# Kernel optimization log

Hardware: AMD Instinct MI355X
Metric: run time of the kernel (lower is better)

## Reference

```python
import jax, jax.numpy as jnp
import numpy as np

INPUT_SIZE = 256
N_DIM = 128
BATCH = 1024


def setup_inputs() -> dict:
    key = jax.random.key(0)
    ks = jax.random.split(key, 8)
    X = jax.random.normal(ks[0], (BATCH, INPUT_SIZE), dtype=jnp.float32)
    h = jax.random.normal(ks[1], (BATCH, INPUT_SIZE * N_DIM), dtype=jnp.float32)
    W_r = jax.random.normal(ks[2], (INPUT_SIZE, 1, N_DIM), dtype=jnp.float32)
    W_z = jax.random.normal(ks[3], (INPUT_SIZE, 1, N_DIM), dtype=jnp.float32)
    W_h = jax.random.normal(ks[4], (INPUT_SIZE, 1, N_DIM), dtype=jnp.float32)
    # orthogonal init for U (matches nn.init.orthogonal_ in spirit)
    def ortho(k):
        a = jax.random.normal(k, (INPUT_SIZE, N_DIM, N_DIM), dtype=jnp.float32)
        q, _ = jnp.linalg.qr(a)
        return q.astype(jnp.float32)
    U_r = ortho(ks[5])
    U_z = ortho(ks[6])
    U_h = ortho(ks[7])
    b_r = jnp.zeros((INPUT_SIZE, N_DIM), dtype=jnp.float32)
    b_z = jnp.zeros((INPUT_SIZE, N_DIM), dtype=jnp.float32)
    b_h = jnp.zeros((INPUT_SIZE, N_DIM), dtype=jnp.float32)
    return {"X": X, "h": h, "W_r": W_r, "W_z": W_z, "W_h": W_h,
            "U_r": U_r, "U_z": U_z, "U_h": U_h,
            "b_r": b_r, "b_z": b_z, "b_h": b_h}


def reference(X, h, W_r, W_z, W_h, U_r, U_z, U_h, b_r, b_z, b_h):
    B = X.shape[0]
    hg = h.reshape(B, INPUT_SIZE, N_DIM)  # [B, I, D]
    # X contribution: X[b,i] * W[i,0,k] -> [B, I, D]
    xW_r = X[:, :, None] * W_r[:, 0, :][None]
    xW_z = X[:, :, None] * W_z[:, 0, :][None]
    xW_h = X[:, :, None] * W_h[:, 0, :][None]
    # grouped GEMMs: [B,I,D] x [I,D,D] -> [B,I,D]
    r = jax.nn.sigmoid(xW_r + jnp.einsum('bij,ijk->bik', hg, U_r) + b_r)
    z = jax.nn.sigmoid(xW_z + jnp.einsum('bij,ijk->bik', hg, U_z) + b_z)
    h_tilde = jnp.tanh(xW_h + jnp.einsum('bij,ijk->bik', r * hg, U_h) + b_h)
    h_new = z * hg + (1.0 - z) * h_tilde
    return (h_new.reshape(B, INPUT_SIZE * N_DIM),
            h_tilde.reshape(B, INPUT_SIZE * N_DIM))
```

## Files before the change

### kernel.cpp

```cpp
#include <hip/hip_runtime.h>
#include <hip/hip_bf16.h>
#include <stdint.h>

#define I_SIZE 256
#define D_DIM 128
#define BATCH 1024

typedef __attribute__((ext_vector_type(8))) short short8;
typedef __attribute__((ext_vector_type(4))) short short4v;
typedef __attribute__((ext_vector_type(4))) float floatx4;

__device__ inline short f2bf(float f) {
    union { float f; uint32_t u; } v; v.f = f;
    uint32_t u = v.u;
    uint32_t r = (u + 0x7FFFu + ((u >> 16) & 1u)) >> 16;
    return (short)(r & 0xFFFFu);
}
__device__ inline float bf2f(short s) {
    union { uint32_t u; float f; } v; v.u = ((uint32_t)(uint16_t)s) << 16;
    return v.f;
}
__device__ inline uint32_t pkbf(float a, float b) {
    __hip_bfloat162 h = __float22bfloat162_rn(make_float2(a, b));
    union { __hip_bfloat162 h; uint32_t u; } v; v.h = h; return v.u;
}
__device__ inline float sigmoidf_fast(float x) { return 1.0f / (1.0f + __expf(-x)); }
__device__ inline float tanhf_fast(float x)    { return 2.0f / (1.0f + __expf(-2.0f * x)) - 1.0f; }

#define S_H 136

__global__ __launch_bounds__(1024, 4) void gru_fused(
    const float* __restrict__ X, const float* __restrict__ H,
    const float* __restrict__ Wr, const float* __restrict__ Wz, const float* __restrict__ Wh,
    const float* __restrict__ Ur, const float* __restrict__ Uz, const float* __restrict__ Uh,
    const float* __restrict__ br, const float* __restrict__ bz, const float* __restrict__ bh,
    float* __restrict__ out)
{
    __shared__ short Ut[3 * D_DIM * D_DIM];
    __shared__ short hgb[D_DIM * S_H];
    __shared__ float Wl[6][D_DIM];

    const int tid   = threadIdx.x;
    const int group = blockIdx.x;
    const int lane  = tid & 63;
    const int w     = tid >> 6;

    if (tid < D_DIM) {
        Wl[0][tid] = Wr[group * D_DIM + tid];
        Wl[1][tid] = Wz[group * D_DIM + tid];
        Wl[2][tid] = Wh[group * D_DIM + tid];
        Wl[3][tid] = br[group * D_DIM + tid];
        Wl[4][tid] = bz[group * D_DIM + tid];
        Wl[5][tid] = bh[group * D_DIM + tid];
    }

    {
        const int kc = tid & 127;
        const int jb = tid >> 7;
        #pragma unroll
        for (int g = 0; g < 3; ++g) {
            const float* Ug = ((g == 0) ? Ur : (g == 1) ? Uz : Uh)
                              + (size_t)group * (D_DIM * D_DIM);
            short* dst = &Ut[g * (D_DIM * D_DIM)];
            #pragma unroll
            for (int m = 0; m < 4; ++m) {
                const int j0 = m * 8 + jb;
                float a0 = Ug[(4 * j0 + 0) * D_DIM + kc];
                float a1 = Ug[(4 * j0 + 1) * D_DIM + kc];
                float a2 = Ug[(4 * j0 + 2) * D_DIM + kc];
                float a3 = Ug[(4 * j0 + 3) * D_DIM + kc];
                short4v s; s.x = f2bf(a0); s.y = f2bf(a1); s.z = f2bf(a2); s.w = f2bf(a3);
                const int p = (j0 >> 1) ^ (kc & 7);
                *(short4v*)&dst[kc * D_DIM + p * 8 + 4 * (j0 & 1)] = s;
            }
        }
    }

    const int am = lane & 15;
    const int aq = lane >> 4;
    const int rg = w >> 1;
    const int nh = w & 1;
    const int r0 = rg * 16;
    const size_t HOFF = (size_t)BATCH * I_SIZE * D_DIM;
    const int srow = tid >> 3;
    const int scol = (tid & 7) * 4;

    int pswz[4];
    #pragma unroll
    for (int kk = 0; kk < 4; ++kk) pswz[kk] = ((4 * kk + aq) ^ (am & 7)) * 8;

    const floatx4 zero = {0.f, 0.f, 0.f, 0.f};

    for (int pass = 0; pass < 8; ++pass) {
        const int R = pass * 128;

        #pragma unroll
        for (int it = 0; it < 4; ++it) {
            int col = scol + it * 32;
            float4 v = *(const float4*)(H + (size_t)(R + srow) * (I_SIZE * D_DIM)
                                        + group * D_DIM + col);
            uint2 uu; uu.x = pkbf(v.x, v.y); uu.y = pkbf(v.z, v.w);
            *(uint2*)&hgb[srow * S_H + col] = uu;
        }
        __syncthreads();

        short8 a[4];
        #pragma unroll
        for (int kk = 0; kk < 4; ++kk)
            a[kk] = *(const short8*)&hgb[(r0 + am) * S_H + kk * 32 + aq * 8];

        floatx4 accr[4], accz[4];
        #pragma unroll
        for (int t2 = 0; t2 < 4; ++t2) { accr[t2] = zero; accz[t2] = zero; }

        #pragma unroll
        for (int t2 = 0; t2 < 4; ++t2) {
            const int n = nh * 64 + t2 * 16 + am;
            const short* rowp = &Ut[n * D_DIM];
            #pragma unroll
            for (int kk = 0; kk < 4; ++kk)
                accr[t2] = __builtin_amdgcn_mfma_f32_16x16x32_bf16(
                    a[kk], *(const short8*)(rowp + pswz[kk]), accr[t2], 0, 0, 0);
            #pragma unroll
            for (int kk = 0; kk < 4; ++kk)
                accz[t2] = __builtin_amdgcn_mfma_f32_16x16x32_bf16(
                    a[kk], *(const short8*)(rowp + 16384 + pswz[kk]), accz[t2], 0, 0, 0);
        }

        float Xv[4];
        #pragma unroll
        for (int pp = 0; pp < 4; ++pp)
            Xv[pp] = X[(size_t)(R + r0 + aq * 4 + pp) * I_SIZE + group];

        float zr[4][4], hgc[4][4];
        #pragma unroll
        for (int t2 = 0; t2 < 4; ++t2) {
            const int c = nh * 64 + t2 * 16 + am;
            const float wr = Wl[0][c], wz = Wl[1][c], brv = Wl[3][c], bzv = Wl[4][c];
            #pragma unroll
            for (int pp = 0; pp < 4; ++pp) {
                const int rl = r0 + aq * 4 + pp;
                float hgv = bf2f(hgb[rl * S_H + c]);
                float rv = sigmoidf_fast(accr[t2][pp] + Xv[pp] * wr + brv);
                float zv = sigmoidf_fast(accz[t2][pp] + Xv[pp] * wz + bzv);
                zr[t2][pp]  = zv;
                hgc[t2][pp] = hgv;
                hgb[rl * S_H + c] = f2bf(rv * hgv);
            }
        }
        __syncthreads();

        short8 ap[4];
        #pragma unroll
        for (int kk = 0; kk < 4; ++kk)
            ap[kk] = *(const short8*)&hgb[(r0 + am) * S_H + kk * 32 + aq * 8];

        floatx4 acch[4];
        #pragma unroll
        for (int t2 = 0; t2 < 4; ++t2) acch[t2] = zero;
        #pragma unroll
        for (int t2 = 0; t2 < 4; ++t2) {
            const int n = nh * 64 + t2 * 16 + am;
            const short* rowp = &Ut[32768 + n * D_DIM];
            #pragma unroll
            for (int kk = 0; kk < 4; ++kk)
                acch[t2] = __builtin_amdgcn_mfma_f32_16x16x32_bf16(
                    ap[kk], *(const short8*)(rowp + pswz[kk]), acch[t2], 0, 0, 0);
        }

        #pragma unroll
        for (int t2 = 0; t2 < 4; ++t2) {
            const int c = nh * 64 + t2 * 16 + am;
            const float wh = Wl[2][c], bhv = Wl[5][c];
            #pragma unroll
            for (int pp = 0; pp < 4; ++pp) {
                const int rl = r0 + aq * 4 + pp;
                float ht = tanhf_fast(acch[t2][pp] + Xv[pp] * wh + bhv);
                float zv = zr[t2][pp];
                float hn = zv * hgc[t2][pp] + (1.0f - zv) * ht;
                size_t o = (size_t)(R + rl) * (I_SIZE * D_DIM) + group * D_DIM + c;
                out[o]        = hn;
                out[HOFF + o] = ht;
            }
        }
        __syncthreads();
    }
}

extern "C" void kernel_launch(void* const* d_in, const int* in_sizes, int n_in,
                              void* d_out, int out_size, void* d_ws, size_t ws_size,
                              hipStream_t stream) {
    const float* X  = (const float*)d_in[0];
    const float* H  = (const float*)d_in[1];
    const float* Wr = (const float*)d_in[2];
    const float* Wz = (const float*)d_in[3];
    const float* Wh = (const float*)d_in[4];
    const float* Ur = (const float*)d_in[5];
    const float* Uz = (const float*)d_in[6];
    const float* Uh = (const float*)d_in[7];
    const float* br = (const float*)d_in[8];
    const float* bz = (const float*)d_in[9];
    const float* bh = (const float*)d_in[10];

    (void)d_ws; (void)ws_size;

    gru_fused<<<dim3(I_SIZE), dim3(1024), 0, stream>>>(
        X, H, Wr, Wz, Wh, Ur, Uz, Uh, br, bz, bh, (float*)d_out);
}
```

Baseline: 462.2 us.

## Prefetch next H tile into registers and use LDS-only barriers

Loads the next pass's 128 rows of H into registers before the r/z MFMAs, so the global load latency overlaps with compute, and writes them to shared memory at the end of each pass. Caches the block's column of X in shared memory once instead of doing strided global loads every pass. Replaces __syncthreads with an inline-asm barrier that waits only on LDS counters, so outstanding global stores and prefetch loads do not stall the barrier. This raises register pressure through the held float4 prefetch, and the hand-written barrier depends on the compiler placing its vmcnt waits correctly.

```diff
diff --git a/kernel.cpp b/kernel.cpp
--- a/kernel.cpp
+++ b/kernel.cpp
@@ -26,6 +26,8 @@
 }
 __device__ inline float sigmoidf_fast(float x) { return 1.0f / (1.0f + __expf(-x)); }
 __device__ inline float tanhf_fast(float x)    { return 2.0f / (1.0f + __expf(-2.0f * x)) - 1.0f; }
+
+#define BAR_LGKM() asm volatile("s_waitcnt lgkmcnt(0)\n\ts_barrier" ::: "memory")
 
 #define S_H 136
 
@@ -39,6 +41,7 @@
     __shared__ short Ut[3 * D_DIM * D_DIM];
     __shared__ short hgb[D_DIM * S_H];
     __shared__ float Wl[6][D_DIM];
+    __shared__ float Xl[BATCH];
 
     const int tid   = threadIdx.x;
     const int group = blockIdx.x;
@@ -53,6 +56,7 @@
         Wl[4][tid] = bz[group * D_DIM + tid];
         Wl[5][tid] = bh[group * D_DIM + tid];
     }
+    Xl[tid] = X[(size_t)tid * I_SIZE + group];
 
     {
         const int kc = tid & 127;
@@ -76,14 +80,25 @@
         }
     }
 
+    const int srow = tid >> 3;
+    const int scol = (tid & 7) * 4;
+
+    #pragma unroll
+    for (int it = 0; it < 4; ++it) {
+        int col = scol + it * 32;
+        float4 v = *(const float4*)(H + (size_t)srow * (I_SIZE * D_DIM)
+                                    + group * D_DIM + col);
+        uint2 uu; uu.x = pkbf(v.x, v.y); uu.y = pkbf(v.z, v.w);
+        *(uint2*)&hgb[srow * S_H + col] = uu;
+    }
+    BAR_LGKM();
+
     const int am = lane & 15;
     const int aq = lane >> 4;
     const int rg = w >> 1;
     const int nh = w & 1;
     const int r0 = rg * 16;
     const size_t HOFF = (size_t)BATCH * I_SIZE * D_DIM;
-    const int srow = tid >> 3;
-    const int scol = (tid & 7) * 4;
 
     int pswz[4];
     #pragma unroll
@@ -94,20 +109,20 @@
     for (int pass = 0; pass < 8; ++pass) {
         const int R = pass * 128;
 
-        #pragma unroll
-        for (int it = 0; it < 4; ++it) {
-            int col = scol + it * 32;
-            float4 v = *(const float4*)(H + (size_t)(R + srow) * (I_SIZE * D_DIM)
-                                        + group * D_DIM + col);
-            uint2 uu; uu.x = pkbf(v.x, v.y); uu.y = pkbf(v.z, v.w);
-            *(uint2*)&hgb[srow * S_H + col] = uu;
-        }
-        __syncthreads();
-
         short8 a[4];
         #pragma unroll
         for (int kk = 0; kk < 4; ++kk)
             a[kk] = *(const short8*)&hgb[(r0 + am) * S_H + kk * 32 + aq * 8];
+
+        float4 pf[4];
+        if (pass < 7) {
+            #pragma unroll
+            for (int it = 0; it < 4; ++it) {
+                int col = scol + it * 32;
+                pf[it] = *(const float4*)(H + (size_t)(R + 128 + srow) * (I_SIZE * D_DIM)
+                                          + group * D_DIM + col);
+            }
+        }
 
         floatx4 accr[4], accz[4];
         #pragma unroll
@@ -130,7 +145,7 @@
         float Xv[4];
         #pragma unroll
         for (int pp = 0; pp < 4; ++pp)
-            Xv[pp] = X[(size_t)(R + r0 + aq * 4 + pp) * I_SIZE + group];
+            Xv[pp] = Xl[R + r0 + aq * 4 + pp];
 
         float zr[4][4], hgc[4][4];
         #pragma unroll
@@ -148,7 +163,7 @@
                 hgb[rl * S_H + c] = f2bf(rv * hgv);
             }
         }
-        __syncthreads();
+        BAR_LGKM();
 
         short8 ap[4];
         #pragma unroll
@@ -183,7 +198,17 @@
                 out[HOFF + o] = ht;
             }
         }
-        __syncthreads();
+
+        if (pass < 7) {
+            BAR_LGKM();
+            #pragma unroll
+            for (int it = 0; it < 4; ++it) {
+                int col = scol + it * 32;
+                uint2 uu; uu.x = pkbf(pf[it].x, pf[it].y); uu.y = pkbf(pf[it].z, pf[it].w);
+                *(uint2*)&hgb[srow * S_H + col] = uu;
+            }
+            BAR_LGKM();
+        }
     }
 }
 
```

After: 430.7 us. -6.8%, faster.
